# Optimization experiments

Measured on AMD Instinct MI355X. Metric: run time of the kernel, lower is better.

Reference implementation:

```python
import jax, jax.numpy as jnp
import numpy as np

N = 10000      # nodes
DIN = 1024     # input feature dim
H = 256        # hidden dim
NC = 3         # classes
EDGE_P = 0.002 # ~avg degree 20


def _lin(key, fin, fout):
    s = 1.0 / np.sqrt(fin)
    kw, kb = jax.random.split(key)
    W = jax.random.uniform(kw, (fin, fout), jnp.float32, -s, s)
    b = jax.random.uniform(kb, (fout,), jnp.float32, -s, s)
    return W, b


def setup_inputs() -> dict:
    key = jax.random.key(0)
    ks = jax.random.split(key, 10)
    features = jax.random.normal(ks[0], (N, DIN), jnp.float32)
    # sparse weighted adjacency with zero diagonal (dense storage, as the module expects)
    mask = jax.random.uniform(ks[1], (N, N)) < EDGE_P
    wts = jax.random.uniform(ks[2], (N, N), jnp.float32)
    adj = jnp.where(mask, wts, 0.0) * (1.0 - jnp.eye(N, dtype=jnp.float32))
    W0, b0 = _lin(ks[3], DIN, H)
    W1, b1 = _lin(ks[4], H, H)
    W2, b2 = _lin(ks[5], H, H)
    C1w, c1b = _lin(ks[6], 2 * H, H)
    C2w, c2b = _lin(ks[7], H, H // 2)
    C3w, c3b = _lin(ks[8], H // 2, NC)
    return {"features": features, "adj": adj,
            "W0": W0, "b0": b0, "W1": W1, "b1": b1, "W2": W2, "b2": b2,
            "C1w": C1w, "c1b": c1b, "C2w": C2w, "c2b": c2b, "C3w": C3w, "c3b": c3b}


def _gcn_norm(adj):
    # PyG GCNConv: add self-loops (weight 1), symmetric deg^{-1/2} normalization.
    A = adj + jnp.eye(adj.shape[0], dtype=adj.dtype)
    deg = A.sum(axis=1)
    dinv = jnp.where(deg > 0, jax.lax.rsqrt(deg), 0.0)
    return dinv[:, None] * A * dinv[None, :]


def reference(features, adj, W0, b0, W1, b1, W2, b2, C1w, c1b, C2w, c2b, C3w, c3b):
    An = _gcn_norm(adj)                       # [N, N] normalized adjacency
    x = features
    for W, b in ((W0, b0), (W1, b1), (W2, b2)):
        x = jax.nn.relu(An @ (x @ W) + b)     # linear -> aggregate -> bias -> relu
        # dropout is identity in eval mode
    g = jnp.concatenate([x.max(axis=0), x.mean(axis=0)])  # [2H]
    h = jax.nn.relu(g @ C1w + c1b)
    h = jax.nn.relu(h @ C2w + c2b)
    return h @ C3w + c3b                      # [NC] logits
```

## Files before the change

kernel.cpp:

```cpp
#include <hip/hip_runtime.h>
#include <hip/hip_bf16.h>

#define NN 10000
#define FDIN 1024
#define HH 256
#define CAP 64
#define MPAD 10112
#define WT_BLOCKS 1536
#define G1_BLOCKS 316

typedef unsigned short u16;
typedef unsigned int u32;
typedef __attribute__((ext_vector_type(8))) short short8;
typedef __attribute__((ext_vector_type(4))) float f32x4;

__device__ __forceinline__ float ld_in(const void* p, size_t i, int bf) {
    if (bf) {
        unsigned short u = ((const unsigned short*)p)[i];
        return __uint_as_float(((unsigned int)u) << 16);
    }
    return ((const float*)p)[i];
}

__device__ __forceinline__ u16 bf16bits(float x) {
    __hip_bfloat16 h = __float2bfloat16(x);
    return *(u16*)&h;
}

__device__ __forceinline__ float bf16val(u16 u) {
    return __uint_as_float(((unsigned int)u) << 16);
}

__device__ __forceinline__ int local_flag(const void* feat, int tid, int* cnts) {
    u16 u = ((const u16*)feat)[2 * tid];
    int e = (u >> 7) & 0xFF;
    bool pred = (e >= 100 && e <= 137);
    unsigned long long b = __ballot(pred);
    if ((tid & 63) == 0) cnts[tid >> 6] = __popcll(b);
    __syncthreads();
    return (cnts[0] + cnts[1] + cnts[2] + cnts[3]) >= 128;
}

__global__ __launch_bounds__(256) void k_wt(const void* __restrict__ feat,
                                            const void* __restrict__ W0,
                                            const void* __restrict__ W1,
                                            const void* __restrict__ W2,
                                            int* __restrict__ flag,
                                            u16* __restrict__ w0t,
                                            u16* __restrict__ w1t,
                                            u16* __restrict__ w2t) {
    __shared__ int cnts[4];
    int tid = threadIdx.x;
    int f = local_flag(feat, tid, cnts);
    if (blockIdx.x == 0 && tid == 0) *flag = f;
    int idx = blockIdx.x * 256 + tid;
    const void* W; u16* Wt; int K;
    if (idx < FDIN * HH)                { W = W0; Wt = w0t; K = FDIN; }
    else if (idx < FDIN * HH + HH * HH) { W = W1; Wt = w1t; K = HH; idx -= FDIN * HH; }
    else                                { W = W2; Wt = w2t; K = HH; idx -= FDIN * HH + HH * HH; }
    int k = idx >> 8, n = idx & 255;
    Wt[(size_t)n * K + k] = bf16bits(ld_in(W, (size_t)idx, f));
}


__device__ __forceinline__ void lds_store(unsigned char* Asb, unsigned char* Bsb, int tid,
                                          const uint4* sa, const uint4* sb) {
    #pragma unroll
    for (int q = 0; q < 2; ++q) {
        int c = q * 256 + tid, row = c >> 3, b = (c & 7) << 4;
        *(uint4*)(Asb + row * 128 + (b ^ ((row & 7) << 4))) = sa[q];
    }
    #pragma unroll
    for (int q = 0; q < 4; ++q) {
        int c = q * 256 + tid, n = c >> 3, b = (c & 7) << 4;
        *(uint4*)(Bsb + n * 128 + (b ^ ((n & 7) << 4))) = sb[q];
    }
}

__device__ __forceinline__ void compute64(const unsigned char* Asb, const unsigned char* Bsb,
                                          int l, int wm, int wn, f32x4 acc[2][4]) {
    #pragma unroll
    for (int kk = 0; kk < 2; ++kk) {
        int kb = kk * 64 + ((l >> 4) << 4);
        short8 av[2], bv[4];
        #pragma unroll
        for (int i = 0; i < 2; ++i) {
            int row = wm * 32 + i * 16 + (l & 15);
            av[i] = *(const short8*)(Asb + row * 128 + (kb ^ ((row & 7) << 4)));
        }
        #pragma unroll
        for (int j = 0; j < 4; ++j) {
            int n = wn * 64 + j * 16 + (l & 15);
            bv[j] = *(const short8*)(Bsb + n * 128 + (kb ^ ((n & 7) << 4)));
        }
        #pragma unroll
        for (int i = 0; i < 2; ++i)
            #pragma unroll
            for (int j = 0; j < 4; ++j)
                acc[i][j] = __builtin_amdgcn_mfma_f32_16x16x32_bf16(av[i], bv[j], acc[i][j], 0, 0, 0);
    }
}

__device__ __forceinline__ uint4 load_a(const void* A, int f, size_t row, int K, int e0) {
    if (f) return *(const uint4*)((const u16*)A + row * K + e0);
    const float* fp = (const float*)A + row * K + e0;
    float4 v0 = *(const float4*)fp, v1 = *(const float4*)(fp + 4);
    float4 v2 = *(const float4*)(fp + 8), v3 = *(const float4*)(fp + 12);
    float vv[16] = {v0.x, v0.y, v0.z, v0.w, v1.x, v1.y, v1.z, v1.w,
                    v2.x, v2.y, v2.z, v2.w, v3.x, v3.y, v3.z, v3.w};
    u16 o[16];
    #pragma unroll
    for (int e = 0; e < 16; ++e) o[e] = bf16bits(vv[e]);
    return *(const uint4*)o;
}

__device__ __forceinline__ void gemm_body(const void* A, int f, const u16* Bt,
                                          u16* Y, int K, int m0, int n0, int tid,
                                          unsigned char* Asb, unsigned char* Bsb) {
    const int l = tid & 63;
    const int wid = tid >> 6;
    const int wm = wid >> 1, wn = wid & 1;
    f32x4 acc[2][4] = {};
    uint4 sa[2], sb[4], ta[2], tb[4];
    auto g_load = [&](int k0, uint4* xa, uint4* xb) {
        #pragma unroll
        for (int q = 0; q < 2; ++q) {
            int c = q * 256 + tid, row = c >> 3, e0 = (c & 7) << 3;
            uint4 v = {0u, 0u, 0u, 0u};
            if (m0 + row < NN) v = load_a(A, f, (size_t)(m0 + row), K, k0 + e0);
            xa[q] = v;
        }
        #pragma unroll
        for (int q = 0; q < 4; ++q) {
            int c = q * 256 + tid, n = c >> 3, b = (c & 7) << 4;
            xb[q] = *(const uint4*)((const unsigned char*)(Bt + (size_t)(n0 + n) * K + k0) + b);
        }
    };
    g_load(0, sa, sb);
    const int nt = K >> 6;
    for (int t = 0; t < nt; t += 2) {
        __syncthreads();
        lds_store(Asb, Bsb, tid, sa, sb);
        __syncthreads();
        g_load((t + 1) << 6, ta, tb);
        compute64(Asb, Bsb, l, wm, wn, acc);
        __syncthreads();
        lds_store(Asb, Bsb, tid, ta, tb);
        __syncthreads();
        if (t + 2 < nt) g_load((t + 2) << 6, sa, sb);
        compute64(Asb, Bsb, l, wm, wn, acc);
    }
    #pragma unroll
    for (int i = 0; i < 2; ++i) {
        int r0 = m0 + wm * 32 + i * 16 + ((l >> 4) << 2);
        #pragma unroll
        for (int j = 0; j < 4; ++j) {
            int col = n0 + wn * 64 + j * 16 + (l & 15);
            #pragma unroll
            for (int r = 0; r < 4; ++r)
                Y[(size_t)(r0 + r) * HH + col] = bf16bits(acc[i][j][r]);
        }
    }
}

__global__ __launch_bounds__(256) void k_front(const void* __restrict__ feat,
                                               const void* __restrict__ adj,
                                               const u16* __restrict__ w0t,
                                               u16* __restrict__ ybuf,
                                               int* __restrict__ ellc,
                                               float* __restrict__ ellv,
                                               int* __restrict__ cnt,
                                               float* __restrict__ dinv) {
    __shared__ uint4 As4[512];
    __shared__ uint4 Bs4[1024];
    __shared__ int cnts[4];
    __shared__ int s_cnt;
    __shared__ float s_sum;
    int tid = threadIdx.x;
    int bid = blockIdx.x;
    if (tid == 0) { s_cnt = 0; s_sum = 0.f; }
    int f = local_flag(feat, tid, cnts);

    if (bid < G1_BLOCKS) {
        int m0 = (bid >> 1) * 64;
        int n0 = (bid & 1) * 128;
        gemm_body(feat, f, w0t, ybuf, FDIN, m0, n0, tid,
                  (unsigned char*)As4, (unsigned char*)Bs4);
        return;
    }
    int i = bid - G1_BLOCKS;
    float lsum = 0.f;
    if (f) {
        const uint4* p = (const uint4*)((const u16*)adj + (size_t)i * NN);
        for (int t = tid; t < NN / 8; t += 256) {
            uint4 q = p[t];
            if ((q.x | q.y | q.z | q.w) == 0u) continue;
            unsigned int w_[4] = {q.x, q.y, q.z, q.w};
            #pragma unroll
            for (int w = 0; w < 4; ++w) {
                #pragma unroll
                for (int hh = 0; hh < 2; ++hh) {
                    unsigned short u = (unsigned short)(w_[w] >> (16 * hh));
                    if (u) {
                        float v = bf16val(u);
                        lsum += v;
                        int slot = atomicAdd(&s_cnt, 1);
                        if (slot < CAP) {
                            ellc[(size_t)i * CAP + slot] = t * 8 + w * 2 + hh;
                            ellv[(size_t)i * CAP + slot] = v;
                        }
                    }
                }
            }
        }
    } else {
        const uint4* p = (const uint4*)((const float*)adj + (size_t)i * NN);
        for (int t = tid; t < NN / 4; t += 256) {
            uint4 qi = p[t];
            if ((qi.x | qi.y | qi.z | qi.w) == 0u) continue;
            unsigned int w_[4] = {qi.x, qi.y, qi.z, qi.w};
            #pragma unroll
            for (int w = 0; w < 4; ++w) {
                float v = __uint_as_float(w_[w]);
                if (v != 0.f) {
                    lsum += v;
                    int slot = atomicAdd(&s_cnt, 1);
                    if (slot < CAP) {
                        ellc[(size_t)i * CAP + slot] = t * 4 + w;
                        ellv[(size_t)i * CAP + slot] = v;
                    }
                }
            }
        }
    }
    for (int off = 32; off > 0; off >>= 1) lsum += __shfl_down(lsum, off, 64);
    if ((tid & 63) == 0) atomicAdd(&s_sum, lsum);
    __syncthreads();
    if (tid == 0) {
        float deg = s_sum + 1.0f;
        dinv[i] = rsqrtf(deg);
        cnt[i] = s_cnt < CAP ? s_cnt : CAP;
    }
}

__global__ __launch_bounds__(256) void k_mfma(const u16* __restrict__ A,
                                              const u16* __restrict__ Bt,
                                              u16* __restrict__ Y, int K) {
    __shared__ uint4 As4[512];
    __shared__ uint4 Bs4[1024];
    int tid = threadIdx.x;
    int m0 = blockIdx.y * 64;
    int n0 = blockIdx.x * 128;
    gemm_body(A, 1, Bt, Y, K, m0, n0, tid,
              (unsigned char*)As4, (unsigned char*)Bs4);
}

__global__ __launch_bounds__(128) void k_agg(const u32* __restrict__ y,
                                             const int* __restrict__ ellc,
                                             const float* __restrict__ ellv,
                                             const int* __restrict__ cnt,
                                             const float* __restrict__ dinv,
                                             const void* __restrict__ bias,
                                             const int* __restrict__ flag,
                                             u32* __restrict__ xout) {
    int i = blockIdx.x, j = threadIdx.x;
    int f = *flag;
    float di = dinv[i];
    u32 w = y[(size_t)i * 128 + j];
    float a0 = di * bf16val((u16)(w & 0xffff));
    float a1 = di * bf16val((u16)(w >> 16));
    int c_ = cnt[i];
    for (int e = 0; e < c_; ++e) {
        int c = ellc[(size_t)i * CAP + e];
        float s = ellv[(size_t)i * CAP + e] * dinv[c];
        u32 v = y[(size_t)c * 128 + j];
        a0 = fmaf(s, bf16val((u16)(v & 0xffff)), a0);
        a1 = fmaf(s, bf16val((u16)(v >> 16)), a1);
    }
    float v0 = fmaf(di, a0, ld_in(bias, (size_t)(2 * j), f));
    float v1 = fmaf(di, a1, ld_in(bias, (size_t)(2 * j + 1), f));
    v0 = v0 > 0.f ? v0 : 0.f;
    v1 = v1 > 0.f ? v1 : 0.f;
    xout[(size_t)i * 128 + j] = (u32)bf16bits(v0) | ((u32)bf16bits(v1) << 16);
}

__global__ __launch_bounds__(256) void k_pool(const u16* __restrict__ x,
                                              float* __restrict__ pmax,
                                              float* __restrict__ psum) {
    int j = threadIdx.x, b = blockIdx.x;
    int r0 = b * 250;
    float m = 0.f, s = 0.f;
    for (int r = r0; r < r0 + 250; ++r) {
        float v = bf16val(x[(size_t)r * HH + j]);
        m = fmaxf(m, v);
        s += v;
    }
    pmax[b * HH + j] = m;
    psum[b * HH + j] = s;
}

__global__ __launch_bounds__(256) void k_head(const float* __restrict__ pmax,
                                              const float* __restrict__ psum,
                                              const void* C1w, const void* c1b,
                                              const void* C2w, const void* c2b,
                                              const void* C3w, const void* c3b,
                                              const int* __restrict__ flag,
                                              void* __restrict__ out) {
    __shared__ float gs[2 * HH], h1[HH], h2[HH / 2];
    int j = threadIdx.x;
    int f = *flag;
    float m = 0.f, s = 0.f;
    #pragma unroll 4
    for (int b = 0; b < 40; ++b) {
        m = fmaxf(m, pmax[b * HH + j]);
        s += psum[b * HH + j];
    }
    gs[j] = m;
    gs[HH + j] = s * (1.0f / (float)NN);
    __syncthreads();
    float a = 0.f;
    for (int k = 0; k < 2 * HH; ++k) a = fmaf(gs[k], ld_in(C1w, (size_t)k * HH + j, f), a);
    a += ld_in(c1b, j, f);
    h1[j] = a > 0.f ? a : 0.f;
    __syncthreads();
    if (j < HH / 2) {
        float b2_ = 0.f;
        for (int k = 0; k < HH; ++k) b2_ = fmaf(h1[k], ld_in(C2w, (size_t)k * (HH / 2) + j, f), b2_);
        b2_ += ld_in(c2b, j, f);
        h2[j] = b2_ > 0.f ? b2_ : 0.f;
    }
    __syncthreads();
    if (j < 3) {
        float o = 0.f;
        for (int k = 0; k < HH / 2; ++k) o = fmaf(h2[k], ld_in(C3w, (size_t)k * 3 + j, f), o);
        o += ld_in(c3b, j, f);
        if (f) ((__hip_bfloat16*)out)[j] = __float2bfloat16(o);
        else   ((float*)out)[j] = o;
    }
}

extern "C" void kernel_launch(void* const* d_in, const int* in_sizes, int n_in,
                              void* d_out, int out_size, void* d_ws, size_t ws_size,
                              hipStream_t stream) {
    const void* feat = d_in[0];
    const void* adj  = d_in[1];
    const void* W0 = d_in[2];  const void* b0 = d_in[3];
    const void* W1 = d_in[4];  const void* b1 = d_in[5];
    const void* W2 = d_in[6];  const void* b2 = d_in[7];
    const void* C1w = d_in[8]; const void* c1b = d_in[9];
    const void* C2w = d_in[10]; const void* c2b = d_in[11];
    const void* C3w = d_in[12]; const void* c3b = d_in[13];

    char* ws = (char*)d_ws;
    size_t o = 0;
    auto take = [&](size_t bytes) -> void* {
        void* p = ws + o;
        o += (bytes + 255) & ~(size_t)255;
        return p;
    };
    int*   flag  = (int*)take(4);
    float* dinv  = (float*)take((size_t)NN * 4);
    int*   cnt   = (int*)take((size_t)NN * 4);
    int*   ellc  = (int*)take((size_t)NN * CAP * 4);
    float* ellv  = (float*)take((size_t)NN * CAP * 4);
    u16*   w0t   = (u16*)take((size_t)HH * FDIN * 2);
    u16*   w1t   = (u16*)take((size_t)HH * HH * 2);
    u16*   w2t   = (u16*)take((size_t)HH * HH * 2);
    u16*   xbuf  = (u16*)take((size_t)MPAD * HH * 2);
    u16*   ybuf  = (u16*)take((size_t)MPAD * HH * 2);
    float* pmax  = (float*)take((size_t)40 * HH * 4);
    float* psum  = (float*)take((size_t)40 * HH * 4);

    k_wt<<<WT_BLOCKS, 256, 0, stream>>>(feat, W0, W1, W2, flag, w0t, w1t, w2t);
    k_front<<<G1_BLOCKS + NN, 256, 0, stream>>>(feat, adj, w0t, ybuf,
                                                ellc, ellv, cnt, dinv);

    dim3 gg(2, MPAD / 64);
    k_agg<<<NN, 128, 0, stream>>>((const u32*)ybuf, ellc, ellv, cnt, dinv, b0, flag, (u32*)xbuf);
    k_mfma<<<gg, 256, 0, stream>>>(xbuf, w1t, ybuf, HH);
    k_agg<<<NN, 128, 0, stream>>>((const u32*)ybuf, ellc, ellv, cnt, dinv, b1, flag, (u32*)xbuf);
    k_mfma<<<gg, 256, 0, stream>>>(xbuf, w2t, ybuf, HH);
    k_agg<<<NN, 128, 0, stream>>>((const u32*)ybuf, ellc, ellv, cnt, dinv, b2, flag, (u32*)xbuf);

    k_pool<<<40, 256, 0, stream>>>(xbuf, pmax, psum);
    k_head<<<1, 256, 0, stream>>>(pmax, psum, C1w, c1b, C2w, c2b, C3w, c3b, flag, d_out);
}
```

Before: 410.7 us.

## Fuse adjacency scan into weight transpose kernel and shrink GEMM tiles

The adjacency scan to ELL is moved into the weight-transpose kernel, and the first feature GEMM becomes a separate launch instead of sharing a grid with the scan. GEMM tiles shrink from 64 to 32 rows, so each wave handles one 16-row MFMA strip and the grid doubles, which should raise occupancy for the small-K layers. The aggregation kernel now processes two nodes per 256-thread block. In exchange, each block reuses less of the B tile, and the big GEMM can no longer overlap the adjacency scan.

```diff
diff --git a/kernel.cpp b/kernel.cpp
--- a/kernel.cpp
+++ b/kernel.cpp
@@ -7,7 +7,6 @@
 #define CAP 64
 #define MPAD 10112
 #define WT_BLOCKS 1536
-#define G1_BLOCKS 316
 
 typedef unsigned short u16;
 typedef unsigned int u32;
@@ -41,19 +40,85 @@
     return (cnts[0] + cnts[1] + cnts[2] + cnts[3]) >= 128;
 }
 
-__global__ __launch_bounds__(256) void k_wt(const void* __restrict__ feat,
-                                            const void* __restrict__ W0,
-                                            const void* __restrict__ W1,
-                                            const void* __restrict__ W2,
-                                            int* __restrict__ flag,
-                                            u16* __restrict__ w0t,
-                                            u16* __restrict__ w1t,
-                                            u16* __restrict__ w2t) {
+__global__ __launch_bounds__(256) void k_scanwt(const void* __restrict__ feat,
+                                                const void* __restrict__ adj,
+                                                const void* __restrict__ W0,
+                                                const void* __restrict__ W1,
+                                                const void* __restrict__ W2,
+                                                int* __restrict__ flag,
+                                                int* __restrict__ ellc,
+                                                float* __restrict__ ellv,
+                                                int* __restrict__ cnt,
+                                                float* __restrict__ dinv,
+                                                u16* __restrict__ w0t,
+                                                u16* __restrict__ w1t,
+                                                u16* __restrict__ w2t) {
     __shared__ int cnts[4];
+    __shared__ int s_cnt;
+    __shared__ float s_sum;
     int tid = threadIdx.x;
+    int bid = blockIdx.x;
+    if (tid == 0) { s_cnt = 0; s_sum = 0.f; }
     int f = local_flag(feat, tid, cnts);
-    if (blockIdx.x == 0 && tid == 0) *flag = f;
-    int idx = blockIdx.x * 256 + tid;
+    if (bid == 0 && tid == 0) *flag = f;
+
+    if (bid < NN) {
+        int i = bid;
+        float lsum = 0.f;
+        if (f) {
+            const uint4* p = (const uint4*)((const u16*)adj + (size_t)i * NN);
+            for (int t = tid; t < NN / 8; t += 256) {
+                uint4 q = p[t];
+                if ((q.x | q.y | q.z | q.w) == 0u) continue;
+                unsigned int w_[4] = {q.x, q.y, q.z, q.w};
+                #pragma unroll
+                for (int w = 0; w < 4; ++w) {
+                    #pragma unroll
+                    for (int hh = 0; hh < 2; ++hh) {
+                        unsigned short u = (unsigned short)(w_[w] >> (16 * hh));
+                        if (u) {
+                            float v = bf16val(u);
+                            lsum += v;
+                            int slot = atomicAdd(&s_cnt, 1);
+                            if (slot < CAP) {
+                                ellc[(size_t)i * CAP + slot] = t * 8 + w * 2 + hh;
+                                ellv[(size_t)i * CAP + slot] = v;
+                            }
+                        }
+                    }
+                }
+            }
+        } else {
+            const uint4* p = (const uint4*)((const float*)adj + (size_t)i * NN);
+            for (int t = tid; t < NN / 4; t += 256) {
+                uint4 qi = p[t];
+                if ((qi.x | qi.y | qi.z | qi.w) == 0u) continue;
+                unsigned int w_[4] = {qi.x, qi.y, qi.z, qi.w};
+                #pragma unroll
+                for (int w = 0; w < 4; ++w) {
+                    float v = __uint_as_float(w_[w]);
+                    if (v != 0.f) {
+                        lsum += v;
+                        int slot = atomicAdd(&s_cnt, 1);
+                        if (slot < CAP) {
+                            ellc[(size_t)i * CAP + slot] = t * 4 + w;
+                            ellv[(size_t)i * CAP + slot] = v;
+                        }
+                    }
+                }
+            }
+        }
+        for (int off = 32; off > 0; off >>= 1) lsum += __shfl_down(lsum, off, 64);
+        if ((tid & 63) == 0) atomicAdd(&s_sum, lsum);
+        __syncthreads();
+        if (tid == 0) {
+            float deg = s_sum + 1.0f;
+            dinv[i] = rsqrtf(deg);
+            cnt[i] = s_cnt < CAP ? s_cnt : CAP;
+        }
+        return;
+    }
+    int idx = (bid - NN) * 256 + tid;
     const void* W; u16* Wt; int K;
     if (idx < FDIN * HH)                { W = W0; Wt = w0t; K = FDIN; }
     else if (idx < FDIN * HH + HH * HH) { W = W1; Wt = w1t; K = HH; idx -= FDIN * HH; }
@@ -62,44 +127,6 @@
     Wt[(size_t)n * K + k] = bf16bits(ld_in(W, (size_t)idx, f));
 }
 
-
-__device__ __forceinline__ void lds_store(unsigned char* Asb, unsigned char* Bsb, int tid,
-                                          const uint4* sa, const uint4* sb) {
-    #pragma unroll
-    for (int q = 0; q < 2; ++q) {
-        int c = q * 256 + tid, row = c >> 3, b = (c & 7) << 4;
-        *(uint4*)(Asb + row * 128 + (b ^ ((row & 7) << 4))) = sa[q];
-    }
-    #pragma unroll
-    for (int q = 0; q < 4; ++q) {
-        int c = q * 256 + tid, n = c >> 3, b = (c & 7) << 4;
-        *(uint4*)(Bsb + n * 128 + (b ^ ((n & 7) << 4))) = sb[q];
-    }
-}
-
-__device__ __forceinline__ void compute64(const unsigned char* Asb, const unsigned char* Bsb,
-                                          int l, int wm, int wn, f32x4 acc[2][4]) {
-    #pragma unroll
-    for (int kk = 0; kk < 2; ++kk) {
-        int kb = kk * 64 + ((l >> 4) << 4);
-        short8 av[2], bv[4];
-        #pragma unroll
-        for (int i = 0; i < 2; ++i) {
-            int row = wm * 32 + i * 16 + (l & 15);
-            av[i] = *(const short8*)(Asb + row * 128 + (kb ^ ((row & 7) << 4)));
-        }
-        #pragma unroll
-        for (int j = 0; j < 4; ++j) {
-            int n = wn * 64 + j * 16 + (l & 15);
-            bv[j] = *(const short8*)(Bsb + n * 128 + (kb ^ ((n & 7) << 4)));
-        }
-        #pragma unroll
-        for (int i = 0; i < 2; ++i)
-            #pragma unroll
-            for (int j = 0; j < 4; ++j)
-                acc[i][j] = __builtin_amdgcn_mfma_f32_16x16x32_bf16(av[i], bv[j], acc[i][j], 0, 0, 0);
-    }
-}
 
 __device__ __forceinline__ uint4 load_a(const void* A, int f, size_t row, int K, int e0) {
     if (f) return *(const uint4*)((const u16*)A + row * K + e0);
@@ -114,21 +141,49 @@
     return *(const uint4*)o;
 }
 
+__device__ __forceinline__ void lds_store(unsigned char* Asb, unsigned char* Bsb, int tid,
+                                          uint4 sa, const uint4* sb) {
+    {
+        int row = tid >> 3, b = (tid & 7) << 4;
+        *(uint4*)(Asb + row * 128 + (b ^ ((row & 7) << 4))) = sa;
+    }
+    #pragma unroll
+    for (int q = 0; q < 4; ++q) {
+        int c = q * 256 + tid, n = c >> 3, b = (c & 7) << 4;
+        *(uint4*)(Bsb + n * 128 + (b ^ ((n & 7) << 4))) = sb[q];
+    }
+}
+
+__device__ __forceinline__ void compute64(const unsigned char* Asb, const unsigned char* Bsb,
+                                          int l, int wm, int wn, f32x4 acc[4]) {
+    #pragma unroll
+    for (int kk = 0; kk < 2; ++kk) {
+        int kb = kk * 64 + ((l >> 4) << 4);
+        int row = wm * 16 + (l & 15);
+        short8 av = *(const short8*)(Asb + row * 128 + (kb ^ ((row & 7) << 4)));
+        #pragma unroll
+        for (int j = 0; j < 4; ++j) {
+            int n = wn * 64 + j * 16 + (l & 15);
+            short8 bv = *(const short8*)(Bsb + n * 128 + (kb ^ ((n & 7) << 4)));
+            acc[j] = __builtin_amdgcn_mfma_f32_16x16x32_bf16(av, bv, acc[j], 0, 0, 0);
+        }
+    }
+}
+
 __device__ __forceinline__ void gemm_body(const void* A, int f, const u16* Bt,
                                           u16* Y, int K, int m0, int n0, int tid,
                                           unsigned char* Asb, unsigned char* Bsb) {
     const int l = tid & 63;
     const int wid = tid >> 6;
     const int wm = wid >> 1, wn = wid & 1;
-    f32x4 acc[2][4] = {};
-    uint4 sa[2], sb[4], ta[2], tb[4];
-    auto g_load = [&](int k0, uint4* xa, uint4* xb) {
-        #pragma unroll
-        for (int q = 0; q < 2; ++q) {
-            int c = q * 256 + tid, row = c >> 3, e0 = (c & 7) << 3;
+    f32x4 acc[4] = {};
+    uint4 sa, sb[4], ta, tb[4];
+    auto g_load = [&](int k0, uint4& xa, uint4* xb) {
+        {
+            int row = tid >> 3, e0 = (tid & 7) << 3;
             uint4 v = {0u, 0u, 0u, 0u};
             if (m0 + row < NN) v = load_a(A, f, (size_t)(m0 + row), K, k0 + e0);
-            xa[q] = v;
+            xa = v;
         }
         #pragma unroll
         for (int q = 0; q < 4; ++q) {
@@ -150,112 +205,32 @@
         if (t + 2 < nt) g_load((t + 2) << 6, sa, sb);
         compute64(Asb, Bsb, l, wm, wn, acc);
     }
+    int r0 = m0 + wm * 16 + ((l >> 4) << 2);
     #pragma unroll
-    for (int i = 0; i < 2; ++i) {
-        int r0 = m0 + wm * 32 + i * 16 + ((l >> 4) << 2);
+    for (int j = 0; j < 4; ++j) {
+        int col = n0 + wn * 64 + j * 16 + (l & 15);
         #pragma unroll
-        for (int j = 0; j < 4; ++j) {
-            int col = n0 + wn * 64 + j * 16 + (l & 15);
-            #pragma unroll
-            for (int r = 0; r < 4; ++r)
-                Y[(size_t)(r0 + r) * HH + col] = bf16bits(acc[i][j][r]);
-        }
-    }
-}
-
-__global__ __launch_bounds__(256) void k_front(const void* __restrict__ feat,
-                                               const void* __restrict__ adj,
-                                               const u16* __restrict__ w0t,
-                                               u16* __restrict__ ybuf,
-                                               int* __restrict__ ellc,
-                                               float* __restrict__ ellv,
-                                               int* __restrict__ cnt,
-                                               float* __restrict__ dinv) {
-    __shared__ uint4 As4[512];
-    __shared__ uint4 Bs4[1024];
-    __shared__ int cnts[4];
-    __shared__ int s_cnt;
-    __shared__ float s_sum;
-    int tid = threadIdx.x;
-    int bid = blockIdx.x;
-    if (tid == 0) { s_cnt = 0; s_sum = 0.f; }
-    int f = local_flag(feat, tid, cnts);
-
-    if (bid < G1_BLOCKS) {
-        int m0 = (bid >> 1) * 64;
-        int n0 = (bid & 1) * 128;
-        gemm_body(feat, f, w0t, ybuf, FDIN, m0, n0, tid,
-                  (unsigned char*)As4, (unsigned char*)Bs4);
-        return;
-    }
-    int i = bid - G1_BLOCKS;
-    float lsum = 0.f;
-    if (f) {
-        const uint4* p = (const uint4*)((const u16*)adj + (size_t)i * NN);
-        for (int t = tid; t < NN / 8; t += 256) {
-            uint4 q = p[t];
-            if ((q.x | q.y | q.z | q.w) == 0u) continue;
-            unsigned int w_[4] = {q.x, q.y, q.z, q.w};
-            #pragma unroll
-            for (int w = 0; w < 4; ++w) {
-                #pragma unroll
-                for (int hh = 0; hh < 2; ++hh) {
-                    unsigned short u = (unsigned short)(w_[w] >> (16 * hh));
-                    if (u) {
-                        float v = bf16val(u);
-                        lsum += v;
-                        int slot = atomicAdd(&s_cnt, 1);
-                        if (slot < CAP) {
-                            ellc[(size_t)i * CAP + slot] = t * 8 + w * 2 + hh;
-                            ellv[(size_t)i * CAP + slot] = v;
-                        }
-                    }
-                }
-            }
-        }
-    } else {
-        const uint4* p = (const uint4*)((const float*)adj + (size_t)i * NN);
-        for (int t = tid; t < NN / 4; t += 256) {
-            uint4 qi = p[t];
-            if ((qi.x | qi.y | qi.z | qi.w) == 0u) continue;
-            unsigned int w_[4] = {qi.x, qi.y, qi.z, qi.w};
-            #pragma unroll
-            for (int w = 0; w < 4; ++w) {
-                float v = __uint_as_float(w_[w]);
-                if (v != 0.f) {
-                    lsum += v;
-                    int slot = atomicAdd(&s_cnt, 1);
-                    if (slot < CAP) {
-                        ellc[(size_t)i * CAP + slot] = t * 4 + w;
-                        ellv[(size_t)i * CAP + slot] = v;
-                    }
-                }
-            }
-        }
-    }
-    for (int off = 32; off > 0; off >>= 1) lsum += __shfl_down(lsum, off, 64);
-    if ((tid & 63) == 0) atomicAdd(&s_sum, lsum);
-    __syncthreads();
-    if (tid == 0) {
-        float deg = s_sum + 1.0f;
-        dinv[i] = rsqrtf(deg);
-        cnt[i] = s_cnt < CAP ? s_cnt : CAP;
-    }
-}
-
-__global__ __launch_bounds__(256) void k_mfma(const u16* __restrict__ A,
+        for (int r = 0; r < 4; ++r)
+            Y[(size_t)(r0 + r) * HH + col] = bf16bits(acc[j][r]);
+    }
+}
+
+__global__ __launch_bounds__(256) void k_mfma(const void* __restrict__ A,
                                               const u16* __restrict__ Bt,
+                                              const int* __restrict__ flag,
+                                              int f_mode,
                                               u16* __restrict__ Y, int K) {
-    __shared__ uint4 As4[512];
+    __shared__ uint4 As4[256];
     __shared__ uint4 Bs4[1024];
     int tid = threadIdx.x;
-    int m0 = blockIdx.y * 64;
+    int f = f_mode ? *flag : 1;
+    int m0 = blockIdx.y * 32;
     int n0 = blockIdx.x * 128;
-    gemm_body(A, 1, Bt, Y, K, m0, n0, tid,
+    gemm_body(A, f, Bt, Y, K, m0, n0, tid,
               (unsigned char*)As4, (unsigned char*)Bs4);
 }
 
-__global__ __launch_bounds__(128) void k_agg(const u32* __restrict__ y,
+__global__ __launch_bounds__(256) void k_agg(const u32* __restrict__ y,
                                              const int* __restrict__ ellc,
                                              const float* __restrict__ ellv,
                                              const int* __restrict__ cnt,
@@ -263,7 +238,8 @@
                                              const void* __restrict__ bias,
                                              const int* __restrict__ flag,
                                              u32* __restrict__ xout) {
-    int i = blockIdx.x, j = threadIdx.x;
+    int i = blockIdx.x * 2 + (threadIdx.x >> 7);
+    int j = threadIdx.x & 127;
     int f = *flag;
     float di = dinv[i];
     u32 w = y[(size_t)i * 128 + j];
@@ -371,16 +347,16 @@
     float* pmax  = (float*)take((size_t)40 * HH * 4);
     float* psum  = (float*)take((size_t)40 * HH * 4);
 
-    k_wt<<<WT_BLOCKS, 256, 0, stream>>>(feat, W0, W1, W2, flag, w0t, w1t, w2t);
-    k_front<<<G1_BLOCKS + NN, 256, 0, stream>>>(feat, adj, w0t, ybuf,
-                                                ellc, ellv, cnt, dinv);
-
-    dim3 gg(2, MPAD / 64);
-    k_agg<<<NN, 128, 0, stream>>>((const u32*)ybuf, ellc, ellv, cnt, dinv, b0, flag, (u32*)xbuf);
-    k_mfma<<<gg, 256, 0, stream>>>(xbuf, w1t, ybuf, HH);
-    k_agg<<<NN, 128, 0, stream>>>((const u32*)ybuf, ellc, ellv, cnt, dinv, b1, flag, (u32*)xbuf);
-    k_mfma<<<gg, 256, 0, stream>>>(xbuf, w2t, ybuf, HH);
-    k_agg<<<NN, 128, 0, stream>>>((const u32*)ybuf, ellc, ellv, cnt, dinv, b2, flag, (u32*)xbuf);
+    k_scanwt<<<NN + WT_BLOCKS, 256, 0, stream>>>(feat, adj, W0, W1, W2, flag,
+                                                 ellc, ellv, cnt, dinv, w0t, w1t, w2t);
+
+    dim3 gg(2, MPAD / 32);
+    k_mfma<<<gg, 256, 0, stream>>>(feat, w0t, flag, 1, ybuf, FDIN);
+    k_agg<<<NN / 2, 256, 0, stream>>>((const u32*)ybuf, ellc, ellv, cnt, dinv, b0, flag, (u32*)xbuf);
+    k_mfma<<<gg, 256, 0, stream>>>(xbuf, w1t, flag, 0, ybuf, HH);
+    k_agg<<<NN / 2, 256, 0, stream>>>((const u32*)ybuf, ellc, ellv, cnt, dinv, b1, flag, (u32*)xbuf);
+    k_mfma<<<gg, 256, 0, stream>>>(xbuf, w2t, flag, 0, ybuf, HH);
+    k_agg<<<NN / 2, 256, 0, stream>>>((const u32*)ybuf, ellc, ellv, cnt, dinv, b2, flag, (u32*)xbuf);
 
     k_pool<<<40, 256, 0, stream>>>(xbuf, pmax, psum);
     k_head<<<1, 256, 0, stream>>>(pmax, psum, C1w, c1b, C2w, c2b, C3w, c3b, flag, d_out);
```

New measurement: 456.2 us. 1.11x slower.
